# Performance work log

Hardware: AMD Instinct MI355X
Metric: run time of the kernel (lower is better)

## Reference

```python
import jax, jax.numpy as jnp
import numpy as np

U = 1  # init kwarg: num_partitions = 2*u + 1 = 3
B, T, N, C = 64, 128, 21, 256


def setup_inputs() -> dict:
    key = jax.random.key(0)
    x = jax.random.normal(key, (B, T, N, C), dtype=jnp.float32)
    return {"x": x}


def _partition_shifts(num_channels, u):
    """Replicates the TF layer's split sizes and per-partition time shifts."""
    num_partitions = 2 * u + 1
    base, rem = divmod(num_channels, num_partitions)
    sizes = [base + 1] * rem + [base] * (num_partitions - rem)
    sizes = [s for s in sizes if s > 0]
    n = len(sizes)
    shifts = []
    for i in range(n):
        if n % 2 == 1:
            shift = i - (n - 1) // 2
        else:
            shift = i - u
            if i >= n // 2 and u > n // 2 - 1:
                shift = i - (n // 2 - 1)
        shifts.append(shift)
    return sizes, shifts


def _temporal_shift(x, u):
    c = x.shape[-1]
    sizes, shifts = _partition_shifts(c, u)
    if len(sizes) <= 1:
        return x
    starts = np.cumsum([0] + sizes)
    parts = []
    for i, s in enumerate(shifts):
        p = x[..., starts[i]:starts[i + 1]]  # [B, T, N, c_i]
        if s > 0:   # shift content toward later time, zero-pad the front
            p = jnp.pad(p[:, :-s], ((0, 0), (s, 0), (0, 0), (0, 0)))
        elif s < 0:  # shift content toward earlier time, zero-pad the end
            p = jnp.pad(p[:, -s:], ((0, 0), (0, -s), (0, 0), (0, 0)))
        parts.append(p)
    return jnp.concatenate(parts, axis=-1)


def reference(x):
    return _temporal_shift(x, U)
```

## Files before the change

kernel.cpp:

```cpp
#include <hip/hip_runtime.h>


#define NT_T 128
#define NT_N 21
#define NT_C 256
#define T_STRIDE_F  (NT_N * NT_C)
#define T_STRIDE_V  (T_STRIDE_F / 4)

__global__ __launch_bounds__(256) void temporal_shift_kernel(
    const float4* __restrict__ xv, float4* __restrict__ ov, int total_vec)
{
    int i = blockIdx.x * blockDim.x + threadIdx.x;
    if (i >= total_vec) return;

    int c4  = i & 63;
    int row = i >> 6;
    int t   = (row / NT_N) & (NT_T - 1);

    if (c4 != 21 && c4 != 42) {
        int s = (c4 <= 20) ? -1 : ((c4 <= 41) ? 0 : 1);
        int ts = t - s;
        if (ts >= 0 && ts < NT_T) {
            ov[i] = xv[i - s * T_STRIDE_V];
        } else {
            ov[i] = make_float4(0.f, 0.f, 0.f, 0.f);
        }
    } else {
        const float* xf = (const float*)xv;
        float* of = (float*)ov;
        int base = i << 2;
        #pragma unroll
        for (int k = 0; k < 4; ++k) {
            int c = (c4 << 2) + k;
            int s = (c < 86) ? -1 : ((c < 171) ? 0 : 1);
            int ts = t - s;
            of[base + k] = (ts >= 0 && ts < NT_T)
                           ? xf[base + k - s * T_STRIDE_F]
                           : 0.f;
        }
    }
}

extern "C" void kernel_launch(void* const* d_in, const int* in_sizes, int n_in,
                              void* d_out, int out_size, void* d_ws, size_t ws_size,
                              hipStream_t stream)
{
    const float4* x = (const float4*)d_in[0];
    float4* out = (float4*)d_out;
    int total_vec = out_size / 4;
    int block = 256;
    int grid = (total_vec + block - 1) / block;
    temporal_shift_kernel<<<grid, block, 0, stream>>>(x, out, total_vec);
}
```

Measured before the change: 296.3 us.

## Map one block per time row with vectorized boundary blends and nontemporal stores

Restructures the grid so each block handles one (batch, time) row, which removes the integer division used to recover the time index. The two partition-boundary vectors now use vectorized loads from neighbouring rows blended per lane instead of scalar per-float loads. Stores become nontemporal to avoid polluting cache on a streaming copy. Out-of-range rows load from a safe offset and zero the result, which adds a redundant read on edge rows.

```diff
diff --git a/kernel.cpp b/kernel.cpp
--- a/kernel.cpp
+++ b/kernel.cpp
@@ -1,42 +1,53 @@
 #include <hip/hip_runtime.h>
 
 
-#define NT_T 128
-#define NT_N 21
-#define NT_C 256
-#define T_STRIDE_F  (NT_N * NT_C)
-#define T_STRIDE_V  (T_STRIDE_F / 4)
+typedef float v4f __attribute__((ext_vector_type(4)));
 
-__global__ __launch_bounds__(256) void temporal_shift_kernel(
-    const float4* __restrict__ xv, float4* __restrict__ ov, int total_vec)
+#define NT_T   128
+#define NT_N   21
+#define NT_C   256
+#define ROW_V  (NT_N * NT_C / 4)
+#define BLOCK  448
+#define ITERS  3
+
+__global__ __launch_bounds__(BLOCK) void temporal_shift_kernel(
+    const v4f* __restrict__ xv, v4f* __restrict__ ov)
 {
-    int i = blockIdx.x * blockDim.x + threadIdx.x;
-    if (i >= total_vec) return;
+    const int bt   = blockIdx.x;
+    const int t    = bt & (NT_T - 1);
+    const int base = bt * ROW_V + threadIdx.x;
+    const int c4   = threadIdx.x & 63;
 
-    int c4  = i & 63;
-    int row = i >> 6;
-    int t   = (row / NT_N) & (NT_T - 1);
+    const v4f zero = {0.f, 0.f, 0.f, 0.f};
 
-    if (c4 != 21 && c4 != 42) {
-        int s = (c4 <= 20) ? -1 : ((c4 <= 41) ? 0 : 1);
-        int ts = t - s;
-        if (ts >= 0 && ts < NT_T) {
-            ov[i] = xv[i - s * T_STRIDE_V];
-        } else {
-            ov[i] = make_float4(0.f, 0.f, 0.f, 0.f);
+    if (c4 == 21) {
+        #pragma unroll
+        for (int k = 0; k < ITERS; ++k) {
+            const int i = base + k * BLOCK;
+            v4f va = (t < NT_T - 1) ? xv[i + ROW_V] : zero;
+            v4f vb = xv[i];
+            v4f r = {va.x, va.y, vb.z, vb.w};
+            __builtin_nontemporal_store(r, &ov[i]);
+        }
+    } else if (c4 == 42) {
+        #pragma unroll
+        for (int k = 0; k < ITERS; ++k) {
+            const int i = base + k * BLOCK;
+            v4f vb = xv[i];
+            v4f vc = (t > 0) ? xv[i - ROW_V] : zero;
+            v4f r = {vb.x, vb.y, vb.z, vc.w};
+            __builtin_nontemporal_store(r, &ov[i]);
         }
     } else {
-        const float* xf = (const float*)xv;
-        float* of = (float*)ov;
-        int base = i << 2;
+        const int  s     = (c4 <= 20) ? -1 : ((c4 <= 41) ? 0 : 1);
+        const bool valid = ((unsigned)(t - s)) < (unsigned)NT_T;
+        const int  off   = valid ? -s * ROW_V : 0;
         #pragma unroll
-        for (int k = 0; k < 4; ++k) {
-            int c = (c4 << 2) + k;
-            int s = (c < 86) ? -1 : ((c < 171) ? 0 : 1);
-            int ts = t - s;
-            of[base + k] = (ts >= 0 && ts < NT_T)
-                           ? xf[base + k - s * T_STRIDE_F]
-                           : 0.f;
+        for (int k = 0; k < ITERS; ++k) {
+            const int i = base + k * BLOCK;
+            v4f v = xv[i + off];
+            v4f r = valid ? v : zero;
+            __builtin_nontemporal_store(r, &ov[i]);
         }
     }
 }
@@ -45,10 +56,8 @@
                               void* d_out, int out_size, void* d_ws, size_t ws_size,
                               hipStream_t stream)
 {
-    const float4* x = (const float4*)d_in[0];
-    float4* out = (float4*)d_out;
-    int total_vec = out_size / 4;
-    int block = 256;
-    int grid = (total_vec + block - 1) / block;
-    temporal_shift_kernel<<<grid, block, 0, stream>>>(x, out, total_vec);
+    const v4f* x = (const v4f*)d_in[0];
+    v4f* out = (v4f*)d_out;
+    const int grid = 64 * NT_T;
+    temporal_shift_kernel<<<grid, BLOCK, 0, stream>>>(x, out);
 }
```

Result: slower. 311.4 us (+5.1%).
